# Performance work log

Measured on AMD Instinct MI355X. Metric: run time of the kernel, lower is better.

## Reference

```python
import jax, jax.numpy as jnp
import numpy as np

B, S, D = 32, 4096, 64          # batch, max seq len, input_dim
P, STRIDE, H = 8, 4, 512        # patch_size, patch_stride, hidden_size
T = (S - P) // STRIDE + 1       # static max token count (sample 0 has length S)
EPS = 1e-6


def setup_inputs() -> dict:
    key = jax.random.key(0)
    k1, k2, k3 = jax.random.split(key, 3)
    x = jax.random.normal(k1, (B, S, D), dtype=jnp.float32)
    lengths = jax.random.randint(k2, (B,), P, S + 1)
    lengths = lengths.at[0].set(S)  # at least one full-length sample -> max_tokens == T
    W = jax.random.normal(k3, (P * D, H), dtype=jnp.float32) / np.sqrt(P * D)
    b = jnp.zeros((H,), dtype=jnp.float32)
    scale = jnp.ones((H,), dtype=jnp.float32)  # RMSNorm scale
    return {"x": x, "lengths": lengths, "W": W, "b": b, "scale": scale}


def _patch(x, lengths):
    # number of tokens per sample: len(range(0, max(L-P+1, 1), STRIDE))
    n_tok = jnp.where(lengths >= P, (lengths - P) // STRIDE + 1, 1)  # [B]
    # gather positions for every (token, within-patch) slot
    pos = jnp.arange(T)[:, None] * STRIDE + jnp.arange(P)[None, :]   # [T, P]
    tokens = x[:, pos, :]                                            # [B, T, P, D]
    valid = (pos[None, :, :] < lengths[:, None, None]) \
          & (jnp.arange(T)[None, :, None] < n_tok[:, None, None])    # [B, T, P]
    tokens = jnp.where(valid[..., None], tokens, 0.0)
    return tokens.reshape(B, T, P * D), n_tok


def reference(x, lengths, W, b, scale):
    tokens, token_lengths = _patch(x, lengths)        # [B, T, P*D], [B]
    h = tokens @ W + b                                # proj -> [B, T, H]
    rms = jnp.sqrt(jnp.mean(h * h, axis=-1, keepdims=True) + EPS)
    hidden = h / rms * scale                          # RMSNorm
    return hidden, token_lengths, tokens
```

## Files before the change

kernel.cpp:

```cpp
#include <hip/hip_runtime.h>
#include <hip/hip_bf16.h>

constexpr int Bc = 32, Sc = 4096, Dc = 64, Pc = 8, STRIDEc = 4, Hc = 512;
constexpr int Tc = (Sc - Pc) / STRIDEc + 1;
constexpr int Kc = Pc * Dc;
constexpr float EPSc = 1e-6f;

typedef __bf16 bf16x8 __attribute__((ext_vector_type(8)));
typedef unsigned short ushort8 __attribute__((ext_vector_type(8)));
typedef float f32x4 __attribute__((ext_vector_type(4)));
typedef unsigned int uint4v __attribute__((ext_vector_type(4)));

__device__ __forceinline__ int n_tok_of(int len) {
    return (len >= Pc) ? ((len - Pc) / STRIDEc + 1) : 1;
}

__device__ __forceinline__ unsigned short f2bf(float f) {
    unsigned u = __builtin_bit_cast(unsigned, f);
    u = (u + 0x7FFFu + ((u >> 16) & 1u)) >> 16;
    return (unsigned short)u;
}
__device__ __forceinline__ unsigned pk2bf(float lo, float hi) {
    return (unsigned)f2bf(lo) | ((unsigned)f2bf(hi) << 16);
}

__global__ __launch_bounds__(256) void prep_kernel(
        const float* __restrict__ W, const int* __restrict__ lengths,
        unsigned short* __restrict__ Wfrag, float* __restrict__ out_tl) {
    __shared__ float tile[32][33];
    const int k0 = blockIdx.x * 32, n0 = blockIdx.y * 32;
    const int r = threadIdx.x >> 3, c = (threadIdx.x & 7) * 4;
    const float4 v = *(const float4*)(W + (size_t)(k0 + r) * Hc + n0 + c);
    tile[c + 0][r] = v.x;
    tile[c + 1][r] = v.y;
    tile[c + 2][r] = v.z;
    tile[c + 3][r] = v.w;
    __syncthreads();
    ushort4 o;
    o.x = f2bf(tile[r][c + 0]);
    o.y = f2bf(tile[r][c + 1]);
    o.z = f2bf(tile[r][c + 2]);
    o.w = f2bf(tile[r][c + 3]);
    const int n   = n0 + r;
    const int kk  = k0 + c;
    const int wv  = n >> 7;
    const int ct  = (n >> 4) & 7;
    const int l15 = n & 15;
    const int stp = kk >> 5;
    const int qd  = (kk >> 3) & 3;
    const size_t off =
        ((((size_t)stp * 4 + wv) * 8 + ct) * 64 + qd * 16 + l15) * 8 + (kk & 7);
    *(ushort4*)(Wfrag + off) = o;
    if (blockIdx.x == 0 && blockIdx.y == 0 && threadIdx.x < Bc)
        out_tl[threadIdx.x] = (float)n_tok_of(lengths[threadIdx.x]);
}

__global__ __launch_bounds__(256, 2) void fused_kernel(
        const float* __restrict__ x, const int* __restrict__ lengths,
        const unsigned short* __restrict__ Wfrag, const float* __restrict__ bias,
        const float* __restrict__ scale, float* __restrict__ hidden,
        float* __restrict__ tokens) {
    const int b  = blockIdx.y;
    const int t0 = blockIdx.x * 64;
    const int len = lengths[b];
    const int ntok = n_tok_of(len);

    __shared__ float ssbuf[4][64];

    const int tid  = threadIdx.x;
    const int w    = tid >> 6;
    const int lane = tid & 63;
    const int l15  = lane & 15;
    const int quad = lane >> 4;

    f32x4 acc[4][8];
#pragma unroll
    for (int tt = 0; tt < 4; ++tt)
#pragma unroll
        for (int ct = 0; ct < 8; ++ct) acc[tt][ct] = (f32x4){0.f, 0.f, 0.f, 0.f};

    const float* xb   = x + (size_t)b * (Sc * Dc);
    float*       tokb = tokens + (size_t)b * Tc * Kc;

    int a_r[2], a_c[2];
#pragma unroll
    for (int it = 0; it < 2; ++it) {
        const int l = tid + it * 256;
        a_r[it] = l >> 3;
        a_c[it] = (l & 7) * 4;
    }
    int ft[4];
#pragma unroll
    for (int tt = 0; tt < 4; ++tt) ft[tt] = t0 + tt * 16 + l15;

    const unsigned short* wf = Wfrag + ((size_t)w * 8) * 512 + (size_t)lane * 8;

    for (int step = 0; step < 16; ++step) {
        const int k0 = step * 32;

#pragma unroll
        for (int it = 0; it < 2; ++it) {
            const int t = t0 + a_r[it];
            const int kk = k0 + a_c[it];
            const int pos = t * STRIDEc + (kk >> 6);
            float4 v = make_float4(0.f, 0.f, 0.f, 0.f);
            if (t < ntok && pos < len)
                v = *(const float4*)(xb + (size_t)t * (STRIDEc * Dc) + kk);
            if (t < Tc)
                *(float4*)(tokb + (size_t)t * Kc + kk) = v;
        }

        ushort8 aW[8];
        const unsigned short* wfs = wf + (size_t)step * (4 * 8 * 512);
#pragma unroll
        for (int ct = 0; ct < 8; ++ct)
            aW[ct] = *(const ushort8*)(wfs + ct * 512);

        bf16x8 btok[4];
        const int kf = k0 + quad * 8;
        const int pf = kf >> 6;
#pragma unroll
        for (int tt = 0; tt < 4; ++tt) {
            const int t = ft[tt];
            float4 f0 = make_float4(0.f, 0.f, 0.f, 0.f);
            float4 f1 = make_float4(0.f, 0.f, 0.f, 0.f);
            if (t < ntok && (t * STRIDEc + pf) < len) {
                const float* src = xb + (size_t)t * (STRIDEc * Dc) + kf;
                f0 = *(const float4*)(src);
                f1 = *(const float4*)(src + 4);
            }
            uint4v uu;
            uu[0] = pk2bf(f0.x, f0.y);
            uu[1] = pk2bf(f0.z, f0.w);
            uu[2] = pk2bf(f1.x, f1.y);
            uu[3] = pk2bf(f1.z, f1.w);
            btok[tt] = __builtin_bit_cast(bf16x8, uu);
        }

#pragma unroll
        for (int ct = 0; ct < 8; ++ct) {
            const bf16x8 av = __builtin_bit_cast(bf16x8, aW[ct]);
#pragma unroll
            for (int tt = 0; tt < 4; ++tt)
                acc[tt][ct] = __builtin_amdgcn_mfma_f32_16x16x32_bf16(
                    av, btok[tt], acc[tt][ct], 0, 0, 0);
        }
    }

    float ss[4] = {0.f, 0.f, 0.f, 0.f};
#pragma unroll
    for (int ct = 0; ct < 8; ++ct) {
        const f32x4 b4 = *(const f32x4*)(bias + w * 128 + ct * 16 + quad * 4);
#pragma unroll
        for (int tt = 0; tt < 4; ++tt) {
            f32x4 h = acc[tt][ct] + b4;
            acc[tt][ct] = h;
            ss[tt] += h[0] * h[0] + h[1] * h[1] + h[2] * h[2] + h[3] * h[3];
        }
    }
#pragma unroll
    for (int tt = 0; tt < 4; ++tt) {
        float s = ss[tt];
        s += __shfl_xor(s, 16);
        s += __shfl_xor(s, 32);
        if (quad == 0) ssbuf[w][tt * 16 + l15] = s;
    }
    __syncthreads();
    float rstd[4];
#pragma unroll
    for (int tt = 0; tt < 4; ++tt) {
        const int r = tt * 16 + l15;
        const float tot = ssbuf[0][r] + ssbuf[1][r] + ssbuf[2][r] + ssbuf[3][r];
        rstd[tt] = rsqrtf(tot * (1.0f / (float)Hc) + EPSc);
    }
#pragma unroll
    for (int ct = 0; ct < 8; ++ct) {
        const f32x4 s4 = *(const f32x4*)(scale + w * 128 + ct * 16 + quad * 4);
#pragma unroll
        for (int tt = 0; tt < 4; ++tt) {
            const int t = ft[tt];
            if (t < Tc) {
                f32x4 o = acc[tt][ct] * rstd[tt] * s4;
                *(f32x4*)(hidden + ((size_t)b * Tc + t) * Hc
                          + w * 128 + ct * 16 + quad * 4) = o;
            }
        }
    }
}

extern "C" void kernel_launch(void* const* d_in, const int* in_sizes, int n_in,
                              void* d_out, int out_size, void* d_ws, size_t ws_size,
                              hipStream_t stream) {
    const float* x       = (const float*)d_in[0];
    const int*   lengths = (const int*)d_in[1];
    const float* W       = (const float*)d_in[2];
    const float* bias    = (const float*)d_in[3];
    const float* scale   = (const float*)d_in[4];

    const size_t BTH = (size_t)Bc * Tc * Hc;
    float* out    = (float*)d_out;
    float* hidden = out;
    float* tl     = out + BTH;
    float* tokens = out + BTH + Bc;

    unsigned short* Wfrag = (unsigned short*)d_ws;

    {
        dim3 grid(Hc / 32, Hc / 32);
        prep_kernel<<<grid, 256, 0, stream>>>(W, lengths, Wfrag, tl);
    }
    {
        dim3 grid(16, Bc);
        fused_kernel<<<grid, 256, 0, stream>>>(x, lengths, Wfrag, bias, scale,
                                               hidden, tokens);
    }
}
```

Before: 210.9 us.

## Split token materialization into separate kernel and shrink GEMM tiles with x prefetch

Moves the tokens output write out of the fused GEMM+RMSNorm kernel into a standalone streaming copy kernel. The GEMM kernel now handles 32 tokens per block instead of 64, targets 3 blocks per CU, and double-buffers the x fragment loads one K-step ahead. The aim is more parallelism and latency hiding in the GEMM. In exchange it adds a kernel launch, and the W fragments are now re-read by twice as many blocks.

After: 240.9 us. 1.14x slower.

```diff
diff --git a/kernel.cpp b/kernel.cpp
--- a/kernel.cpp
+++ b/kernel.cpp
@@ -22,6 +22,25 @@
 }
 __device__ __forceinline__ unsigned pk2bf(float lo, float hi) {
     return (unsigned)f2bf(lo) | ((unsigned)f2bf(hi) << 16);
+}
+
+__global__ __launch_bounds__(256) void tokens_kernel(
+        const float* __restrict__ x, const int* __restrict__ lengths,
+        float* __restrict__ out_tokens) {
+    const int idx = blockIdx.x * 256 + threadIdx.x;
+    const int row = idx >> 7;
+    const int c4  = idx & 127;
+    const int b = row / Tc;
+    const int t = row - b * Tc;
+    const int len = lengths[b];
+    const int ntok = n_tok_of(len);
+    const int p = c4 >> 4;
+    const int pos = t * STRIDEc + p;
+
+    float4 v = make_float4(0.f, 0.f, 0.f, 0.f);
+    if (t < ntok && pos < len)
+        v = *(const float4*)(x + (size_t)b * Sc * Dc + (size_t)t * (STRIDEc * Dc) + c4 * 4);
+    *(float4*)(out_tokens + (size_t)row * Kc + c4 * 4) = v;
 }
 
 __global__ __launch_bounds__(256) void prep_kernel(
@@ -55,17 +74,16 @@
         out_tl[threadIdx.x] = (float)n_tok_of(lengths[threadIdx.x]);
 }
 
-__global__ __launch_bounds__(256, 2) void fused_kernel(
+__global__ __launch_bounds__(256, 3) void gemm_rms_kernel(
         const float* __restrict__ x, const int* __restrict__ lengths,
         const unsigned short* __restrict__ Wfrag, const float* __restrict__ bias,
-        const float* __restrict__ scale, float* __restrict__ hidden,
-        float* __restrict__ tokens) {
+        const float* __restrict__ scale, float* __restrict__ hidden) {
     const int b  = blockIdx.y;
-    const int t0 = blockIdx.x * 64;
+    const int t0 = blockIdx.x * 32;
     const int len = lengths[b];
     const int ntok = n_tok_of(len);
 
-    __shared__ float ssbuf[4][64];
+    __shared__ float ssbuf[4][32];
 
     const int tid  = threadIdx.x;
     const int w    = tid >> 6;
@@ -73,42 +91,42 @@
     const int l15  = lane & 15;
     const int quad = lane >> 4;
 
-    f32x4 acc[4][8];
-#pragma unroll
-    for (int tt = 0; tt < 4; ++tt)
+    f32x4 acc[2][8];
+#pragma unroll
+    for (int tt = 0; tt < 2; ++tt)
 #pragma unroll
         for (int ct = 0; ct < 8; ++ct) acc[tt][ct] = (f32x4){0.f, 0.f, 0.f, 0.f};
 
-    const float* xb   = x + (size_t)b * (Sc * Dc);
-    float*       tokb = tokens + (size_t)b * Tc * Kc;
-
-    int a_r[2], a_c[2];
-#pragma unroll
-    for (int it = 0; it < 2; ++it) {
-        const int l = tid + it * 256;
-        a_r[it] = l >> 3;
-        a_c[it] = (l & 7) * 4;
-    }
-    int ft[4];
-#pragma unroll
-    for (int tt = 0; tt < 4; ++tt) ft[tt] = t0 + tt * 16 + l15;
+    const float* xb = x + (size_t)b * (Sc * Dc);
+    const int ft[2] = {t0 + l15, t0 + 16 + l15};
 
     const unsigned short* wf = Wfrag + ((size_t)w * 8) * 512 + (size_t)lane * 8;
 
+    float4 xf[2][2][2];
+
+#define LOAD_X(buf, stp)                                                     \
+    {                                                                        \
+        const int kf = (stp) * 32 + quad * 8;                                \
+        const int pf = kf >> 6;                                              \
+        _Pragma("unroll")                                                    \
+        for (int tt = 0; tt < 2; ++tt) {                                     \
+            const int t = ft[tt];                                            \
+            float4 f0 = make_float4(0.f, 0.f, 0.f, 0.f);                     \
+            float4 f1 = make_float4(0.f, 0.f, 0.f, 0.f);                     \
+            if (t < ntok && (t * STRIDEc + pf) < len) {                      \
+                const float* src = xb + (size_t)t * (STRIDEc * Dc) + kf;     \
+                f0 = *(const float4*)(src);                                  \
+                f1 = *(const float4*)(src + 4);                              \
+            }                                                                \
+            xf[buf][tt][0] = f0;                                             \
+            xf[buf][tt][1] = f1;                                             \
+        }                                                                    \
+    }
+
+    LOAD_X(0, 0)
+
     for (int step = 0; step < 16; ++step) {
-        const int k0 = step * 32;
-
-#pragma unroll
-        for (int it = 0; it < 2; ++it) {
-            const int t = t0 + a_r[it];
-            const int kk = k0 + a_c[it];
-            const int pos = t * STRIDEc + (kk >> 6);
-            float4 v = make_float4(0.f, 0.f, 0.f, 0.f);
-            if (t < ntok && pos < len)
-                v = *(const float4*)(xb + (size_t)t * (STRIDEc * Dc) + kk);
-            if (t < Tc)
-                *(float4*)(tokb + (size_t)t * Kc + kk) = v;
-        }
+        const int cur = step & 1;
 
         ushort8 aW[8];
         const unsigned short* wfs = wf + (size_t)step * (4 * 8 * 512);
@@ -116,19 +134,13 @@
         for (int ct = 0; ct < 8; ++ct)
             aW[ct] = *(const ushort8*)(wfs + ct * 512);
 
-        bf16x8 btok[4];
-        const int kf = k0 + quad * 8;
-        const int pf = kf >> 6;
-#pragma unroll
-        for (int tt = 0; tt < 4; ++tt) {
-            const int t = ft[tt];
-            float4 f0 = make_float4(0.f, 0.f, 0.f, 0.f);
-            float4 f1 = make_float4(0.f, 0.f, 0.f, 0.f);
-            if (t < ntok && (t * STRIDEc + pf) < len) {
-                const float* src = xb + (size_t)t * (STRIDEc * Dc) + kf;
-                f0 = *(const float4*)(src);
-                f1 = *(const float4*)(src + 4);
-            }
+        if (step < 15) LOAD_X(cur ^ 1, step + 1)
+
+        bf16x8 btok[2];
+#pragma unroll
+        for (int tt = 0; tt < 2; ++tt) {
+            const float4 f0 = xf[cur][tt][0];
+            const float4 f1 = xf[cur][tt][1];
             uint4v uu;
             uu[0] = pk2bf(f0.x, f0.y);
             uu[1] = pk2bf(f0.z, f0.w);
@@ -141,34 +153,35 @@
         for (int ct = 0; ct < 8; ++ct) {
             const bf16x8 av = __builtin_bit_cast(bf16x8, aW[ct]);
 #pragma unroll
-            for (int tt = 0; tt < 4; ++tt)
+            for (int tt = 0; tt < 2; ++tt)
                 acc[tt][ct] = __builtin_amdgcn_mfma_f32_16x16x32_bf16(
                     av, btok[tt], acc[tt][ct], 0, 0, 0);
         }
     }
-
-    float ss[4] = {0.f, 0.f, 0.f, 0.f};
+#undef LOAD_X
+
+    float ss[2] = {0.f, 0.f};
 #pragma unroll
     for (int ct = 0; ct < 8; ++ct) {
         const f32x4 b4 = *(const f32x4*)(bias + w * 128 + ct * 16 + quad * 4);
 #pragma unroll
-        for (int tt = 0; tt < 4; ++tt) {
+        for (int tt = 0; tt < 2; ++tt) {
             f32x4 h = acc[tt][ct] + b4;
             acc[tt][ct] = h;
             ss[tt] += h[0] * h[0] + h[1] * h[1] + h[2] * h[2] + h[3] * h[3];
         }
     }
 #pragma unroll
-    for (int tt = 0; tt < 4; ++tt) {
+    for (int tt = 0; tt < 2; ++tt) {
         float s = ss[tt];
         s += __shfl_xor(s, 16);
         s += __shfl_xor(s, 32);
         if (quad == 0) ssbuf[w][tt * 16 + l15] = s;
     }
     __syncthreads();
-    float rstd[4];
-#pragma unroll
-    for (int tt = 0; tt < 4; ++tt) {
+    float rstd[2];
+#pragma unroll
+    for (int tt = 0; tt < 2; ++tt) {
         const int r = tt * 16 + l15;
         const float tot = ssbuf[0][r] + ssbuf[1][r] + ssbuf[2][r] + ssbuf[3][r];
         rstd[tt] = rsqrtf(tot * (1.0f / (float)Hc) + EPSc);
@@ -177,7 +190,7 @@
     for (int ct = 0; ct < 8; ++ct) {
         const f32x4 s4 = *(const f32x4*)(scale + w * 128 + ct * 16 + quad * 4);
 #pragma unroll
-        for (int tt = 0; tt < 4; ++tt) {
+        for (int tt = 0; tt < 2; ++tt) {
             const int t = ft[tt];
             if (t < Tc) {
                 f32x4 o = acc[tt][ct] * rstd[tt] * s4;
@@ -206,12 +219,16 @@
     unsigned short* Wfrag = (unsigned short*)d_ws;
 
     {
+        const int total = Bc * Tc * 128;
+        tokens_kernel<<<total / 256, 256, 0, stream>>>(x, lengths, tokens);
+    }
+    {
         dim3 grid(Hc / 32, Hc / 32);
         prep_kernel<<<grid, 256, 0, stream>>>(W, lengths, Wfrag, tl);
     }
     {
-        dim3 grid(16, Bc);
-        fused_kernel<<<grid, 256, 0, stream>>>(x, lengths, Wfrag, bias, scale,
-                                               hidden, tokens);
-    }
-}
+        dim3 grid(32, Bc);
+        gemm_rms_kernel<<<grid, 256, 0, stream>>>(x, lengths, Wfrag, bias, scale,
+                                                  hidden);
+    }
+}
```

## Stage activation and weight tiles through LDS with direct global-to-LDS loads

Applied to the files above, without the earlier changes.

Activation tiles are now converted to bf16 once and written to shared memory, and MFMA operands are read from LDS instead of each lane reloading x from global memory. Weight fragments use a new swizzled layout and are copied straight into LDS with global_load_lds. This removes the duplicate global reads of x and spreads the weight load across waves. In exchange it adds two barriers per k-step with no double buffering, uses more LDS, and drops the occupancy hint from launch bounds.

Result: no change. 214.6 us (+1.7%).

```diff
diff --git a/kernel.cpp b/kernel.cpp
--- a/kernel.cpp
+++ b/kernel.cpp
@@ -5,11 +5,11 @@
 constexpr int Tc = (Sc - Pc) / STRIDEc + 1;
 constexpr int Kc = Pc * Dc;
 constexpr float EPSc = 1e-6f;
+constexpr int APITCH = 40;
 
 typedef __bf16 bf16x8 __attribute__((ext_vector_type(8)));
 typedef unsigned short ushort8 __attribute__((ext_vector_type(8)));
 typedef float f32x4 __attribute__((ext_vector_type(4)));
-typedef unsigned int uint4v __attribute__((ext_vector_type(4)));
 
 __device__ __forceinline__ int n_tok_of(int len) {
     return (len >= Pc) ? ((len - Pc) / STRIDEc + 1) : 1;
@@ -23,6 +23,11 @@
 __device__ __forceinline__ unsigned pk2bf(float lo, float hi) {
     return (unsigned)f2bf(lo) | ((unsigned)f2bf(hi) << 16);
 }
+
+#define GLOAD_LDS16(gp, lp)                                                   \
+    __builtin_amdgcn_global_load_lds(                                         \
+        (const __attribute__((address_space(1))) void*)(gp),                  \
+        (__attribute__((address_space(3))) void*)(lp), 16, 0, 0)
 
 __global__ __launch_bounds__(256) void prep_kernel(
         const float* __restrict__ W, const int* __restrict__ lengths,
@@ -43,19 +48,17 @@
     o.w = f2bf(tile[r][c + 3]);
     const int n   = n0 + r;
     const int kk  = k0 + c;
-    const int wv  = n >> 7;
-    const int ct  = (n >> 4) & 7;
-    const int l15 = n & 15;
-    const int stp = kk >> 5;
-    const int qd  = (kk >> 3) & 3;
-    const size_t off =
-        ((((size_t)stp * 4 + wv) * 8 + ct) * 64 + qd * 16 + l15) * 8 + (kk & 7);
+    const int st  = kk >> 5;
+    const int kg  = (kk >> 3) & 3;
+    const int j   = kk & 7;
+    const int slot = kg ^ ((n >> 1) & 3);
+    const size_t off = (size_t)st * 16384 + (size_t)n * 32 + slot * 8 + j;
     *(ushort4*)(Wfrag + off) = o;
     if (blockIdx.x == 0 && blockIdx.y == 0 && threadIdx.x < Bc)
         out_tl[threadIdx.x] = (float)n_tok_of(lengths[threadIdx.x]);
 }
 
-__global__ __launch_bounds__(256, 2) void fused_kernel(
+__global__ __launch_bounds__(256) void fused_kernel(
         const float* __restrict__ x, const int* __restrict__ lengths,
         const unsigned short* __restrict__ Wfrag, const float* __restrict__ bias,
         const float* __restrict__ scale, float* __restrict__ hidden,
@@ -65,6 +68,8 @@
     const int len = lengths[b];
     const int ntok = n_tok_of(len);
 
+    __shared__ unsigned short As[64 * APITCH];
+    __shared__ unsigned short Bs[512 * 32];
     __shared__ float ssbuf[4][64];
 
     const int tid  = threadIdx.x;
@@ -82,64 +87,54 @@
     const float* xb   = x + (size_t)b * (Sc * Dc);
     float*       tokb = tokens + (size_t)b * Tc * Kc;
 
-    int a_r[2], a_c[2];
-#pragma unroll
-    for (int it = 0; it < 2; ++it) {
-        const int l = tid + it * 256;
-        a_r[it] = l >> 3;
-        a_c[it] = (l & 7) * 4;
-    }
-    int ft[4];
-#pragma unroll
-    for (int tt = 0; tt < 4; ++tt) ft[tt] = t0 + tt * 16 + l15;
-
-    const unsigned short* wf = Wfrag + ((size_t)w * 8) * 512 + (size_t)lane * 8;
+    const unsigned short* a_rd[4];
+#pragma unroll
+    for (int tt = 0; tt < 4; ++tt)
+        a_rd[tt] = As + (tt * 16 + l15) * APITCH + quad * 8;
+    const unsigned short* b_rd[8];
+#pragma unroll
+    for (int ct = 0; ct < 8; ++ct) {
+        const int n = w * 128 + ct * 16 + l15;
+        b_rd[ct] = Bs + n * 32 + (quad ^ ((n >> 1) & 3)) * 8;
+    }
 
     for (int step = 0; step < 16; ++step) {
         const int k0 = step * 32;
+        if (step) __syncthreads();
 
 #pragma unroll
         for (int it = 0; it < 2; ++it) {
-            const int t = t0 + a_r[it];
-            const int kk = k0 + a_c[it];
+            const int l = tid + it * 256;
+            const int r = l >> 3;
+            const int c = (l & 7) * 4;
+            const int t = t0 + r;
+            const int kk = k0 + c;
             const int pos = t * STRIDEc + (kk >> 6);
             float4 v = make_float4(0.f, 0.f, 0.f, 0.f);
             if (t < ntok && pos < len)
                 v = *(const float4*)(xb + (size_t)t * (STRIDEc * Dc) + kk);
             if (t < Tc)
                 *(float4*)(tokb + (size_t)t * Kc + kk) = v;
-        }
-
-        ushort8 aW[8];
-        const unsigned short* wfs = wf + (size_t)step * (4 * 8 * 512);
-#pragma unroll
-        for (int ct = 0; ct < 8; ++ct)
-            aW[ct] = *(const ushort8*)(wfs + ct * 512);
+            ushort4 h4;
+            h4.x = f2bf(v.x); h4.y = f2bf(v.y); h4.z = f2bf(v.z); h4.w = f2bf(v.w);
+            *(ushort4*)(As + r * APITCH + c) = h4;
+        }
+
+        const unsigned short* wstep = Wfrag + (size_t)step * 16384;
+#pragma unroll
+        for (int it = 0; it < 8; ++it) {
+            const int cc = w * 8 + it;
+            GLOAD_LDS16(wstep + (size_t)cc * 512 + lane * 8, Bs + cc * 512);
+        }
+        __syncthreads();
 
         bf16x8 btok[4];
-        const int kf = k0 + quad * 8;
-        const int pf = kf >> 6;
-#pragma unroll
-        for (int tt = 0; tt < 4; ++tt) {
-            const int t = ft[tt];
-            float4 f0 = make_float4(0.f, 0.f, 0.f, 0.f);
-            float4 f1 = make_float4(0.f, 0.f, 0.f, 0.f);
-            if (t < ntok && (t * STRIDEc + pf) < len) {
-                const float* src = xb + (size_t)t * (STRIDEc * Dc) + kf;
-                f0 = *(const float4*)(src);
-                f1 = *(const float4*)(src + 4);
-            }
-            uint4v uu;
-            uu[0] = pk2bf(f0.x, f0.y);
-            uu[1] = pk2bf(f0.z, f0.w);
-            uu[2] = pk2bf(f1.x, f1.y);
-            uu[3] = pk2bf(f1.z, f1.w);
-            btok[tt] = __builtin_bit_cast(bf16x8, uu);
-        }
-
+#pragma unroll
+        for (int tt = 0; tt < 4; ++tt)
+            btok[tt] = __builtin_bit_cast(bf16x8, *(const ushort8*)a_rd[tt]);
 #pragma unroll
         for (int ct = 0; ct < 8; ++ct) {
-            const bf16x8 av = __builtin_bit_cast(bf16x8, aW[ct]);
+            const bf16x8 av = __builtin_bit_cast(bf16x8, *(const ushort8*)b_rd[ct]);
 #pragma unroll
             for (int tt = 0; tt < 4; ++tt)
                 acc[tt][ct] = __builtin_amdgcn_mfma_f32_16x16x32_bf16(
@@ -178,7 +173,7 @@
         const f32x4 s4 = *(const f32x4*)(scale + w * 128 + ct * 16 + quad * 4);
 #pragma unroll
         for (int tt = 0; tt < 4; ++tt) {
-            const int t = ft[tt];
+            const int t = t0 + tt * 16 + l15;
             if (t < Tc) {
                 f32x4 o = acc[tt][ct] * rstd[tt] * s4;
                 *(f32x4*)(hidden + ((size_t)b * Tc + t) * Hc
```
